# Kernel optimization log

Measured on AMD Instinct MI355X. Metric: run time of the kernel, lower is better.

Reference implementation:

```python
import jax, jax.numpy as jnp
import numpy as np

# Constants from the source's eval path
BBOX_STDS = (0.1, 0.1, 0.2, 0.2)   # cfg.TRAIN.BBOX_NORMALIZE_STDS (MEANS are zeros)
PRE_NMS = 300                       # cfg.TEST.RPN_POST_NMS_TOP_N
POST_K = 100                        # cfg.PERSON_NMS (fixed output size; zero-padded)
NMS_THRESH = 0.3
SCORE_THRESH = 0.05


def setup_inputs() -> dict:
    key = jax.random.key(0)
    k1, k2, k3, k4 = jax.random.split(key, 4)
    B, N = 64, 32768
    H = W = 1024.0
    # plausible RPN proposal boxes inside the image
    xy = jax.random.uniform(k1, (B, N, 2)) * (W - 160.0)
    wh = jax.random.uniform(k2, (B, N, 2)) * 120.0 + 8.0
    boxes = jnp.concatenate([xy, xy + wh], axis=-1)          # [B,N,4] x1y1x2y2
    cls_prob = jax.random.uniform(k3, (B, N, 2))              # softmax probs [bg, person]
    box_deltas = jax.random.normal(k4, (B, N, 4)) * 0.5
    im_info = jnp.tile(jnp.array([H, W, 1.0], jnp.float32), (B, 1))
    return {"cls_prob": cls_prob, "boxes": boxes, "box_deltas": box_deltas, "im_info": im_info}


def _decode_and_clip(boxes, deltas, im_info):
    # bbox_transform_inv with de-normalized deltas, then clip_boxes
    stds = jnp.array(BBOX_STDS, boxes.dtype)
    d = deltas * stds                                         # MEANS are zero
    w = boxes[..., 2] - boxes[..., 0] + 1.0
    h = boxes[..., 3] - boxes[..., 1] + 1.0
    cx = boxes[..., 0] + 0.5 * w
    cy = boxes[..., 1] + 0.5 * h
    pcx = d[..., 0] * w + cx
    pcy = d[..., 1] * h + cy
    pw = jnp.exp(d[..., 2]) * w
    ph = jnp.exp(d[..., 3]) * h
    x1 = pcx - 0.5 * pw
    y1 = pcy - 0.5 * ph
    x2 = pcx + 0.5 * pw
    y2 = pcy + 0.5 * ph
    hmax = im_info[:, 0][:, None] - 1.0   # [B,1]
    wmax = im_info[:, 1][:, None] - 1.0
    x1 = jnp.clip(x1, 0.0, wmax)
    y1 = jnp.clip(y1, 0.0, hmax)
    x2 = jnp.clip(x2, 0.0, wmax)
    y2 = jnp.clip(y2, 0.0, hmax)
    return jnp.stack([x1, y1, x2, y2], axis=-1)               # [B,N,4]


def _nms_single(boxes_i, scores_i):
    # threshold -> sort (top-k) -> greedy NMS -> fixed-size padded output
    valid = scores_i >= SCORE_THRESH
    s = jnp.where(valid, scores_i, -jnp.inf)
    topv, topi = jax.lax.top_k(s, PRE_NMS)                    # descending sort + pre_nms_topN
    b = boxes_i[topi]                                          # [M,4]
    x1, y1, x2, y2 = b[:, 0], b[:, 1], b[:, 2], b[:, 3]
    areas = (x2 - x1 + 1.0) * (y2 - y1 + 1.0)
    xx1 = jnp.maximum(x1[:, None], x1[None, :])
    yy1 = jnp.maximum(y1[:, None], y1[None, :])
    xx2 = jnp.minimum(x2[:, None], x2[None, :])
    yy2 = jnp.minimum(y2[:, None], y2[None, :])
    inter = jnp.maximum(xx2 - xx1 + 1.0, 0.0) * jnp.maximum(yy2 - yy1 + 1.0, 0.0)
    iou = inter / (areas[:, None] + areas[None, :] - inter)    # [M,M]
    iou = jax.lax.stop_gradient(iou)                           # only drives the boolean keep mask
    idx = jnp.arange(PRE_NMS)
    keep0 = jnp.isfinite(topv)                                 # drop below-threshold padding

    def body(i, keep):
        sup = (iou[i] > NMS_THRESH) & (idx > i) & keep[i]
        return keep & ~sup

    keep = jax.lax.fori_loop(0, PRE_NMS, body, keep0)
    # compact kept boxes (in score order) into a fixed [POST_K,4] buffer, zero-padded
    rank = jnp.cumsum(keep) - 1
    dst = jnp.where(keep & (rank < POST_K), rank, POST_K)      # overflow row POST_K is discarded
    out = jnp.zeros((POST_K + 1, 4), b.dtype).at[dst].set(b)
    return out[:POST_K]


def reference(cls_prob, boxes, box_deltas, im_info):
    pred = _decode_and_clip(boxes, box_deltas, im_info)        # [B,N,4]
    scores_person = cls_prob[:, :, 1]                          # person column
    kept = jax.vmap(_nms_single)(pred, scores_person)          # [B,POST_K,4]
    B = pred.shape[0]
    bidx = jnp.broadcast_to(jnp.arange(B, dtype=pred.dtype)[:, None, None], (B, POST_K, 1))
    return jnp.concatenate([bidx, kept], axis=-1)              # [B,POST_K,5] rois
```

## Files before the change

### kernel.cpp

```cpp
#include <hip/hip_runtime.h>
#include <cstdint>
#include <cstddef>

#define PRE_NMS  300
#define POST_K   100
#define NBUCKET  4096
#define CAND_MAX 2048
#define NCHUNK   16
#define SUB      128
#define NWORDS   5
#define KCAP     192
#define KW       3
#define SUP_STRIDE 8
#define NBUK     512
#define MBASE    0xC0800000u
#define NMS_T    0.3f
#define SCORE_T  0.05f
#define FAST_T   0.9875f

typedef unsigned long long u64;

__device__ __forceinline__ float4 decode_box(float4 bo, float4 de,
                                             float wmax, float hmax) {
    float w  = bo.z - bo.x + 1.0f;
    float hh = bo.w - bo.y + 1.0f;
    float cx = bo.x + 0.5f * w;
    float cy = bo.y + 0.5f * hh;
    float pcx = de.x * 0.1f * w + cx;
    float pcy = de.y * 0.1f * hh + cy;
    float pw  = expf(de.z * 0.2f) * w;
    float ph  = expf(de.w * 0.2f) * hh;
    float x1 = fminf(fmaxf(pcx - 0.5f * pw, 0.0f), wmax);
    float y1 = fminf(fmaxf(pcy - 0.5f * ph, 0.0f), hmax);
    float x2 = fminf(fmaxf(pcx + 0.5f * pw, 0.0f), wmax);
    float y2 = fminf(fmaxf(pcy + 0.5f * ph, 0.0f), hmax);
    return make_float4(x1, y1, x2, y2);
}

__global__ __launch_bounds__(256) void scan_kernel(
    const float* __restrict__ cls_prob,
    const float* __restrict__ boxes,
    const float* __restrict__ deltas,
    const float* __restrict__ im_info,
    u64* __restrict__ keyG,
    float4* __restrict__ boxG,
    int* __restrict__ cntG,
    int N)
{
    const int b     = blockIdx.x >> 4;
    const int chunk = blockIdx.x & (NCHUNK - 1);
    const int nq    = N / 2;
    const int per   = (nq + NCHUNK - 1) / NCHUNK;
    const int base  = chunk * per;
    const int end   = min(base + per, nq);

    __shared__ int lcnt;
    __shared__ u64 lk[SUB];
    __shared__ float4 lb[SUB];
    if (threadIdx.x == 0) lcnt = 0;
    __syncthreads();

    const float hmax = im_info[b * 3 + 0] - 1.0f;
    const float wmax = im_info[b * 3 + 1] - 1.0f;
    const float4* cp = (const float4*)(cls_prob + (size_t)b * N * 2);
    for (int q = base + threadIdx.x; q < end; q += 256) {
        float4 v = cp[q];
        #pragma unroll
        for (int h = 0; h < 2; ++h) {
            float s = h ? v.w : v.y;
            if (s >= FAST_T) {
                int pos = atomicAdd(&lcnt, 1);
                if (pos < SUB) {
                    int idx = 2 * q + h;
                    unsigned int m = __float_as_uint(s) ^ 0xFFFFFFFFu;
                    float4 bo = *(const float4*)(boxes  + ((size_t)b * N + idx) * 4);
                    float4 de = *(const float4*)(deltas + ((size_t)b * N + idx) * 4);
                    lk[pos] = ((u64)m << 32) | (unsigned int)idx;
                    lb[pos] = decode_box(bo, de, wmax, hmax);
                }
            }
        }
    }
    __syncthreads();

    const int cnt = lcnt;
    const size_t obase = (size_t)b * NCHUNK + chunk;
    u64* kb = keyG + obase * SUB;
    float4* bbo = boxG + obase * SUB;
    for (int i = threadIdx.x; i < min(cnt, SUB); i += 256) {
        kb[i]  = lk[i];
        bbo[i] = lb[i];
    }
    if (threadIdx.x == 0) cntG[obase] = cnt;
}

__device__ __forceinline__ u64 keep_init_word(int Kv, int w) {
    int rem = Kv - 64 * w;
    if (rem >= 64) return ~0ull;
    if (rem <= 0)  return 0ull;
    return (1ull << rem) - 1ull;
}

__device__ __forceinline__ u64 bits_above(int b) {
    return (b == 63) ? 0ull : (~0ull << (b + 1));
}

__device__ __forceinline__ int key_bucket(u64 key) {
    unsigned int m = (unsigned int)(key >> 32);
    int d = (int)(m - MBASE);
    if (d < 0) return 0;
    int bu = d >> 9;
    return (bu > NBUK - 1) ? (NBUK - 1) : bu;
}

__device__ __forceinline__ float box_area(float4 v) {
    return (v.z - v.x + 1.0f) * (v.w - v.y + 1.0f);
}

__global__ __launch_bounds__(512) void proposal_kernel(
    const float* __restrict__ cls_prob,
    const float* __restrict__ boxes,
    const float* __restrict__ deltas,
    const float* __restrict__ im_info,
    float* __restrict__ out,
    const u64* __restrict__ keyG,
    const float4* __restrict__ boxG,
    const int* __restrict__ cntG,
    int useWS, int N)
{
    const int b   = blockIdx.x;
    const int tid = threadIdx.x;
    const int NT  = 512;

    __shared__ u64 cand[CAND_MAX];
    int* hist4k = (int*)cand;
    int* buk_off = (int*)cand;
    int* buk_cnt = buk_off + NBUK;
    __shared__ float4 bb[PRE_NMS];
    __shared__ u64 supRow[PRE_NMS * SUP_STRIDE];
    u64* skey2 = supRow;
    __shared__ u64 keepw[NWORDS];
    __shared__ int sel[POST_K];
    __shared__ int ws8[8];
    __shared__ int n_out;
    __shared__ int need_full;
    __shared__ int sh_cc;
    __shared__ int sh_ok;
    __shared__ int cand_count;
    __shared__ int cutoff;
    __shared__ int ccnt[NCHUNK], coff[NCHUNK + 1];

    if (tid == 0) { cand_count = 0; need_full = 0; }
    __syncthreads();

    const float4* cp = (const float4*)(cls_prob + (size_t)b * N * 2);
    const int nq = N / 2;
    const float hmax = im_info[b * 3 + 0] - 1.0f;
    const float wmax = im_info[b * 3 + 1] - 1.0f;

    if (useWS && tid < NCHUNK) ccnt[tid] = cntG[b * NCHUNK + tid];
    __syncthreads();
    if (tid == 0) {
        int ok = useWS;
        int tot = 0;
        if (useWS) {
            for (int c = 0; c < NCHUNK; ++c) {
                if (ccnt[c] > SUB) ok = 0;
                coff[c] = tot;
                tot += ccnt[c];
            }
            coff[NCHUNK] = tot;
            if (tot < PRE_NMS || tot > NT) ok = 0;
        }
        sh_ok = ok;
        sh_cc = tot;
    }
    __syncthreads();
    const bool fast = (sh_ok != 0);
    int cc;

    if (fast) {
        cc = sh_cc;
        buk_off[tid] = 0;
        buk_cnt[tid] = 0;
        if (tid < PRE_NMS) bb[tid] = make_float4(0.f, 0.f, 0.f, 0.f);
        __syncthreads();

        const bool have = (tid < cc);
        u64 my = 0; float4 mybox = make_float4(0.f, 0.f, 0.f, 0.f);
        int bu = 0;
        if (have) {
            int ch = 0;
            while (ch < NCHUNK - 1 && coff[ch + 1] <= tid) ++ch;
            size_t p = ((size_t)b * NCHUNK + ch) * SUB + (tid - coff[ch]);
            my = keyG[p];
            mybox = boxG[p];
            bu = key_bucket(my);
            atomicAdd(&buk_off[bu], 1);
        }
        __syncthreads();
        {
            int v = buk_off[tid];
            int lane = tid & 63;
            int incl = v;
            #pragma unroll
            for (int d = 1; d < 64; d <<= 1) {
                int nv = __shfl_up(incl, d, 64);
                if (lane >= d) incl += nv;
            }
            if (lane == 63) ws8[tid >> 6] = incl;
            __syncthreads();
            int woff = 0;
            #pragma unroll
            for (int w = 0; w < 8; ++w)
                if (w < (tid >> 6)) woff += ws8[w];
            __syncthreads();
            buk_off[tid] = woff + incl - v;
        }
        __syncthreads();
        if (have) skey2[buk_off[bu] + atomicAdd(&buk_cnt[bu], 1)] = my;
        __syncthreads();
        if (have) {
            int o = buk_off[bu], n = buk_cnt[bu];
            int r = o;
            for (int t = o; t < o + n; ++t) r += (skey2[t] < my) ? 1 : 0;
            if (r < PRE_NMS) bb[r] = mybox;
        }
        __syncthreads();
    } else {
        for (int q = tid; q < nq; q += NT) {
            float4 v = cp[q];
            #pragma unroll
            for (int h = 0; h < 2; ++h) {
                float s = h ? v.w : v.y;
                if (s >= FAST_T) {
                    int pos = atomicAdd(&cand_count, 1);
                    if (pos < CAND_MAX) {
                        unsigned int m = __float_as_uint(s) ^ 0xFFFFFFFFu;
                        cand[pos] = ((u64)m << 32) | (unsigned int)(2 * q + h);
                    }
                }
            }
        }
        __syncthreads();
        if (cand_count < PRE_NMS) {
            for (int i = tid; i < NBUCKET; i += NT) hist4k[i] = 0;
            __syncthreads();
            for (int q = tid; q < nq; q += NT) {
                float4 v = cp[q];
                if (v.y >= SCORE_T) atomicAdd(&hist4k[min((int)(v.y * (float)NBUCKET), NBUCKET - 1)], 1);
                if (v.w >= SCORE_T) atomicAdd(&hist4k[min((int)(v.w * (float)NBUCKET), NBUCKET - 1)], 1);
            }
            __syncthreads();
            if (tid == 0) {
                int acc = 0, c = 0;
                for (int i = NBUCKET - 1; i >= 0; --i) {
                    acc += hist4k[i];
                    if (acc >= PRE_NMS) { c = i; break; }
                }
                cutoff = c;
                cand_count = 0;
            }
            __syncthreads();
            const int c = cutoff;
            for (int q = tid; q < nq; q += NT) {
                float4 v = cp[q];
                #pragma unroll
                for (int h = 0; h < 2; ++h) {
                    float s = h ? v.w : v.y;
                    if (s >= SCORE_T) {
                        int bu = min((int)(s * (float)NBUCKET), NBUCKET - 1);
                        if (bu >= c) {
                            int pos = atomicAdd(&cand_count, 1);
                            if (pos < CAND_MAX) {
                                unsigned int m = __float_as_uint(s) ^ 0xFFFFFFFFu;
                                cand[pos] = ((u64)m << 32) | (unsigned int)(2 * q + h);
                            }
                        }
                    }
                }
            }
            __syncthreads();
        }
        cc = min(cand_count, CAND_MAX);
        if (tid == 0) sh_cc = cc;
        __syncthreads();
        cc = sh_cc;
        if (tid < PRE_NMS) bb[tid] = make_float4(0.f, 0.f, 0.f, 0.f);
        __syncthreads();
        for (int c2 = tid; c2 < cc; c2 += NT) {
            u64 my = cand[c2];
            int r = 0;
            for (int k = 0; k < cc; ++k) r += (cand[k] < my) ? 1 : 0;
            if (r < PRE_NMS) {
                int idx = (int)(my & 0xFFFFFFFFull);
                float4 bo = *(const float4*)(boxes  + ((size_t)b * N + idx) * 4);
                float4 de = *(const float4*)(deltas + ((size_t)b * N + idx) * 4);
                bb[r] = decode_box(bo, de, wmax, hmax);
            }
        }
        __syncthreads();
    }

    const int Kv = min(cc, PRE_NMS);

    {
        const int lane = tid & 63;
        const int wv   = tid >> 6;
        float4 cb[KW]; float ca[KW];
        #pragma unroll
        for (int g = 0; g < KW; ++g) {
            float4 v = bb[g * 64 + lane];
            cb[g] = v;
            ca[g] = box_area(v);
        }
        for (int i = wv; i < KCAP; i += 8) {
            float4 bi = bb[i];
            float ai = box_area(bi);
            const int wi = i >> 6, bbit = i & 63;
            u64* rp = supRow + (size_t)i * SUP_STRIDE;
            #pragma unroll
            for (int g = 0; g < KW; ++g) {
                u64 word = 0;
                if (g >= wi) {
                    float xx1 = fmaxf(bi.x, cb[g].x);
                    float yy1 = fmaxf(bi.y, cb[g].y);
                    float xx2 = fminf(bi.z, cb[g].z);
                    float yy2 = fminf(bi.w, cb[g].w);
                    float iw = fmaxf(xx2 - xx1 + 1.0f, 0.0f);
                    float ih = fmaxf(yy2 - yy1 + 1.0f, 0.0f);
                    float inter = iw * ih;
                    bool ov = (inter > NMS_T * (ai + ca[g] - inter));
                    u64 bal = __ballot(ov);
                    word = (g == wi) ? (bal & bits_above(bbit)) : bal;
                }
                if (lane == 0) rp[g] = word;
            }
        }
    }
    __syncthreads();

    if (tid < 64) {
        u64 kw0 = keep_init_word(Kv, 0);
        u64 kw1 = keep_init_word(Kv, 1);
        u64 kw2 = keep_init_word(Kv, 2);

        int nk = 0;
        #pragma unroll
        for (int wi = 0; wi < KW; ++wi) {
            if (nk >= POST_K) break;
            u64 w = (wi == 0) ? kw0 : (wi == 1) ? kw1 : kw2;
            while (w != 0ull && nk < POST_K) {
                int b1 = __ffsll(w) - 1;
                u64 w1 = w & bits_above(b1);
                int b2 = (w1 != 0ull) ? (__ffsll(w1) - 1) : -1;
                u64 w2 = (b2 >= 0) ? (w1 & bits_above(b2)) : 0ull;
                int b3 = (w2 != 0ull) ? (__ffsll(w2) - 1) : -1;
                u64 w3 = (b3 >= 0) ? (w2 & bits_above(b3)) : 0ull;
                int b4 = (w3 != 0ull) ? (__ffsll(w3) - 1) : -1;

                const int base = wi * 64;
                const u64* p1 = supRow + (size_t)(base + b1) * SUP_STRIDE;
                const u64* p2 = supRow + (size_t)(base + ((b2 >= 0) ? b2 : b1)) * SUP_STRIDE;
                const u64* p3 = supRow + (size_t)(base + ((b3 >= 0) ? b3 : b1)) * SUP_STRIDE;
                const u64* p4 = supRow + (size_t)(base + ((b4 >= 0) ? b4 : b1)) * SUP_STRIDE;
                u64 a0 = p1[0], a1 = p1[1], a2 = p1[2];
                u64 c0 = p2[0], c1 = p2[1], c2 = p2[2];
                u64 d0 = p3[0], d1 = p3[1], d2 = p3[2];
                u64 e0 = p4[0], e1 = p4[1], e2 = p4[2];

                u64 aw = (wi == 0) ? a0 : (wi == 1) ? a1 : a2;
                u64 cw = (wi == 0) ? c0 : (wi == 1) ? c1 : c2;
                u64 dw = (wi == 0) ? d0 : (wi == 1) ? d1 : d2;

                kw0 &= ~a0; kw1 &= ~a1; kw2 &= ~a2;
                ++nk;
                bool k2 = false, k3 = false;
                if (b2 >= 0 && nk < POST_K && !((aw >> b2) & 1ull)) {
                    kw0 &= ~c0; kw1 &= ~c1; kw2 &= ~c2;
                    ++nk; k2 = true;
                }
                if (b3 >= 0 && nk < POST_K && !((aw >> b3) & 1ull)
                    && !(k2 && ((cw >> b3) & 1ull))) {
                    kw0 &= ~d0; kw1 &= ~d1; kw2 &= ~d2;
                    ++nk; k3 = true;
                }
                if (b4 >= 0 && nk < POST_K && !((aw >> b4) & 1ull)
                    && !(k2 && ((cw >> b4) & 1ull))
                    && !(k3 && ((dw >> b4) & 1ull))) {
                    kw0 &= ~e0; kw1 &= ~e1; kw2 &= ~e2;
                    ++nk;
                }
                int blast = (b4 >= 0) ? b4 : ((b3 >= 0) ? b3 : ((b2 >= 0) ? b2 : b1));
                u64 self = (wi == 0) ? kw0 : (wi == 1) ? kw1 : kw2;
                w = self & bits_above(blast);
            }
        }
        if (tid == 0) {
            keepw[0] = kw0; keepw[1] = kw1; keepw[2] = kw2;
            keepw[3] = 0ull; keepw[4] = 0ull;
            n_out = nk;
            need_full = (nk < POST_K && Kv > KCAP) ? 1 : 0;
        }
    }
    __syncthreads();

    if (need_full) {
        for (int t = tid; t < PRE_NMS * NWORDS; t += NT) {
            int w = t / PRE_NMS;
            int i = t - w * PRE_NMS;
            int jbase = w * 64;
            int jend  = min(jbase + 64, PRE_NMS);
            u64 bits = 0;
            int jstart = max(jbase, i + 1);
            if (jstart < jend) {
                float4 bi = bb[i];
                float ai = box_area(bi);
                for (int j = jstart; j < jend; ++j) {
                    float4 bj = bb[j];
                    float aj = box_area(bj);
                    float xx1 = fmaxf(bi.x, bj.x);
                    float yy1 = fmaxf(bi.y, bj.y);
                    float xx2 = fminf(bi.z, bj.z);
                    float yy2 = fminf(bi.w, bj.w);
                    float iw = fmaxf(xx2 - xx1 + 1.0f, 0.0f);
                    float ih = fmaxf(yy2 - yy1 + 1.0f, 0.0f);
                    float inter = iw * ih;
                    if (inter > NMS_T * (ai + aj - inter)) bits |= (1ull << (j - jbase));
                }
            }
            supRow[i * SUP_STRIDE + w] = bits;
        }
        __syncthreads();
        if (tid == 0) {
            u64 kk[NWORDS];
            #pragma unroll
            for (int w = 0; w < NWORDS; ++w) kk[w] = keep_init_word(Kv, w);
            int nk = 0;
            for (int i = 0; i < PRE_NMS && nk < POST_K; ++i) {
                if ((kk[i >> 6] >> (i & 63)) & 1ull) {
                    const u64* r = supRow + (size_t)i * SUP_STRIDE;
                    #pragma unroll
                    for (int w = 0; w < NWORDS; ++w) kk[w] &= ~r[w];
                    ++nk;
                }
            }
            #pragma unroll
            for (int w = 0; w < NWORDS; ++w) keepw[w] = kk[w];
            n_out = nk;
        }
        __syncthreads();
    }

    if (tid < PRE_NMS) {
        int wi = tid >> 6, bi = tid & 63;
        u64 w = keepw[wi];
        int prefix = 0;
        #pragma unroll
        for (int ww = 0; ww < NWORDS; ++ww)
            if (ww < wi) prefix += __popcll(keepw[ww]);
        prefix += __popcll(w & ((1ull << bi) - 1ull));
        if (((w >> bi) & 1ull) && prefix < POST_K) sel[prefix] = tid;
    }
    __syncthreads();

    if (tid < POST_K) {
        float* op = out + ((size_t)b * POST_K + tid) * 5;
        op[0] = (float)b;
        if (tid < n_out) {
            float4 v = bb[sel[tid]];
            op[1] = v.x; op[2] = v.y; op[3] = v.z; op[4] = v.w;
        } else {
            op[1] = 0.0f; op[2] = 0.0f; op[3] = 0.0f; op[4] = 0.0f;
        }
    }
}

extern "C" void kernel_launch(void* const* d_in, const int* in_sizes, int n_in,
                              void* d_out, int out_size, void* d_ws, size_t ws_size,
                              hipStream_t stream) {
    const float* cls_prob = (const float*)d_in[0];
    const float* boxes    = (const float*)d_in[1];
    const float* deltas   = (const float*)d_in[2];
    const float* im_info  = (const float*)d_in[3];
    float* out = (float*)d_out;

    const int B = in_sizes[3] / 3;
    const int N = in_sizes[0] / (B * 2);

    const size_t nSlots = (size_t)B * NCHUNK * SUB;
    int*    cntG = (int*)d_ws;
    u64*    keyG = (u64*)((char*)d_ws + 16384);
    float4* boxG = (float4*)((char*)d_ws + 16384 + nSlots * sizeof(u64));
    size_t need = 16384 + nSlots * (sizeof(u64) + sizeof(float4));
    int useWS   = (ws_size >= need && B * NCHUNK * (int)sizeof(int) <= 16384) ? 1 : 0;

    if (useWS) {
        scan_kernel<<<B * NCHUNK, 256, 0, stream>>>(cls_prob, boxes, deltas, im_info,
                                                    keyG, boxG, cntG, N);
    }
    proposal_kernel<<<B, 512, 0, stream>>>(cls_prob, boxes, deltas, im_info, out,
                                           keyG, boxG, cntG, useWS, N);
}
```

Baseline: 127.5 us.

## Replace serial greedy NMS scan with parallel fixed-point column iteration

Result: faster. 117.9 us (-7.5%).

```diff
diff --git a/kernel.cpp b/kernel.cpp
--- a/kernel.cpp
+++ b/kernel.cpp
@@ -101,10 +101,6 @@
     return (1ull << rem) - 1ull;
 }
 
-__device__ __forceinline__ u64 bits_above(int b) {
-    return (b == 63) ? 0ull : (~0ull << (b + 1));
-}
-
 __device__ __forceinline__ int key_bucket(u64 key) {
     unsigned int m = (unsigned int)(key >> 32);
     int d = (int)(m - MBASE);
@@ -139,6 +135,7 @@
     __shared__ float4 bb[PRE_NMS];
     __shared__ u64 supRow[PRE_NMS * SUP_STRIDE];
     u64* skey2 = supRow;
+    u64* colW  = supRow;
     __shared__ u64 keepw[NWORDS];
     __shared__ int sel[POST_K];
     __shared__ int ws8[8];
@@ -314,92 +311,68 @@
             cb[g] = v;
             ca[g] = box_area(v);
         }
-        for (int i = wv; i < KCAP; i += 8) {
-            float4 bi = bb[i];
-            float ai = box_area(bi);
-            const int wi = i >> 6, bbit = i & 63;
-            u64* rp = supRow + (size_t)i * SUP_STRIDE;
+        for (int j = wv; j < KCAP; j += 8) {
+            float4 bj = bb[j];
+            float aj = box_area(bj);
+            const int jw = j >> 6, jb = j & 63;
+            u64* cpw = colW + (size_t)j * 4;
             #pragma unroll
             for (int g = 0; g < KW; ++g) {
                 u64 word = 0;
-                if (g >= wi) {
-                    float xx1 = fmaxf(bi.x, cb[g].x);
-                    float yy1 = fmaxf(bi.y, cb[g].y);
-                    float xx2 = fminf(bi.z, cb[g].z);
-                    float yy2 = fminf(bi.w, cb[g].w);
+                if (g <= jw) {
+                    float xx1 = fmaxf(bj.x, cb[g].x);
+                    float yy1 = fmaxf(bj.y, cb[g].y);
+                    float xx2 = fminf(bj.z, cb[g].z);
+                    float yy2 = fminf(bj.w, cb[g].w);
                     float iw = fmaxf(xx2 - xx1 + 1.0f, 0.0f);
                     float ih = fmaxf(yy2 - yy1 + 1.0f, 0.0f);
                     float inter = iw * ih;
-                    bool ov = (inter > NMS_T * (ai + ca[g] - inter));
+                    bool ov = (inter > NMS_T * (aj + ca[g] - inter));
                     u64 bal = __ballot(ov);
-                    word = (g == wi) ? (bal & bits_above(bbit)) : bal;
-                }
-                if (lane == 0) rp[g] = word;
+                    word = (g == jw) ? (bal & ((1ull << jb) - 1ull)) : bal;
+                }
+                if (lane == 0) cpw[g] = word;
             }
         }
     }
     __syncthreads();
 
     if (tid < 64) {
-        u64 kw0 = keep_init_word(Kv, 0);
-        u64 kw1 = keep_init_word(Kv, 1);
-        u64 kw2 = keep_init_word(Kv, 2);
-
-        int nk = 0;
-        #pragma unroll
-        for (int wi = 0; wi < KW; ++wi) {
-            if (nk >= POST_K) break;
-            u64 w = (wi == 0) ? kw0 : (wi == 1) ? kw1 : kw2;
-            while (w != 0ull && nk < POST_K) {
-                int b1 = __ffsll(w) - 1;
-                u64 w1 = w & bits_above(b1);
-                int b2 = (w1 != 0ull) ? (__ffsll(w1) - 1) : -1;
-                u64 w2 = (b2 >= 0) ? (w1 & bits_above(b2)) : 0ull;
-                int b3 = (w2 != 0ull) ? (__ffsll(w2) - 1) : -1;
-                u64 w3 = (b3 >= 0) ? (w2 & bits_above(b3)) : 0ull;
-                int b4 = (w3 != 0ull) ? (__ffsll(w3) - 1) : -1;
-
-                const int base = wi * 64;
-                const u64* p1 = supRow + (size_t)(base + b1) * SUP_STRIDE;
-                const u64* p2 = supRow + (size_t)(base + ((b2 >= 0) ? b2 : b1)) * SUP_STRIDE;
-                const u64* p3 = supRow + (size_t)(base + ((b3 >= 0) ? b3 : b1)) * SUP_STRIDE;
-                const u64* p4 = supRow + (size_t)(base + ((b4 >= 0) ? b4 : b1)) * SUP_STRIDE;
-                u64 a0 = p1[0], a1 = p1[1], a2 = p1[2];
-                u64 c0 = p2[0], c1 = p2[1], c2 = p2[2];
-                u64 d0 = p3[0], d1 = p3[1], d2 = p3[2];
-                u64 e0 = p4[0], e1 = p4[1], e2 = p4[2];
-
-                u64 aw = (wi == 0) ? a0 : (wi == 1) ? a1 : a2;
-                u64 cw = (wi == 0) ? c0 : (wi == 1) ? c1 : c2;
-                u64 dw = (wi == 0) ? d0 : (wi == 1) ? d1 : d2;
-
-                kw0 &= ~a0; kw1 &= ~a1; kw2 &= ~a2;
-                ++nk;
-                bool k2 = false, k3 = false;
-                if (b2 >= 0 && nk < POST_K && !((aw >> b2) & 1ull)) {
-                    kw0 &= ~c0; kw1 &= ~c1; kw2 &= ~c2;
-                    ++nk; k2 = true;
-                }
-                if (b3 >= 0 && nk < POST_K && !((aw >> b3) & 1ull)
-                    && !(k2 && ((cw >> b3) & 1ull))) {
-                    kw0 &= ~d0; kw1 &= ~d1; kw2 &= ~d2;
-                    ++nk; k3 = true;
-                }
-                if (b4 >= 0 && nk < POST_K && !((aw >> b4) & 1ull)
-                    && !(k2 && ((cw >> b4) & 1ull))
-                    && !(k3 && ((dw >> b4) & 1ull))) {
-                    kw0 &= ~e0; kw1 &= ~e1; kw2 &= ~e2;
-                    ++nk;
-                }
-                int blast = (b4 >= 0) ? b4 : ((b3 >= 0) ? b3 : ((b2 >= 0) ? b2 : b1));
-                u64 self = (wi == 0) ? kw0 : (wi == 1) ? kw1 : kw2;
-                w = self & bits_above(blast);
-            }
-        }
-        if (tid == 0) {
-            keepw[0] = kw0; keepw[1] = kw1; keepw[2] = kw2;
+        const int lane = tid;
+        u64 c00 = colW[(size_t)lane * 4 + 0];
+        u64 c10 = colW[(size_t)(64 + lane) * 4 + 0];
+        u64 c11 = colW[(size_t)(64 + lane) * 4 + 1];
+        u64 c20 = colW[(size_t)(128 + lane) * 4 + 0];
+        u64 c21 = colW[(size_t)(128 + lane) * 4 + 1];
+        u64 c22 = colW[(size_t)(128 + lane) * 4 + 2];
+
+        u64 kv0 = keep_init_word(Kv, 0);
+        u64 kv1 = keep_init_word(Kv, 1);
+        u64 kv2 = keep_init_word(Kv, 2);
+        bool v0 = (kv0 >> lane) & 1ull;
+        bool v1 = (kv1 >> lane) & 1ull;
+        bool v2 = (kv2 >> lane) & 1ull;
+        bool b0 = v0, b1 = v1, b2 = v2;
+
+        for (int it = 0; it < KCAP + 8; ++it) {
+            u64 w0 = __ballot(b0);
+            u64 w1 = __ballot(b1);
+            u64 w2 = __ballot(b2);
+            bool n0 = v0 && (((w0 & c00)) == 0ull);
+            bool n1 = v1 && (((w0 & c10) | (w1 & c11)) == 0ull);
+            bool n2 = v2 && (((w0 & c20) | (w1 & c21) | (w2 & c22)) == 0ull);
+            u64 ch = __ballot(n0 != b0 || n1 != b1 || n2 != b2);
+            b0 = n0; b1 = n1; b2 = n2;
+            if (ch == 0ull) break;
+        }
+        u64 f0 = __ballot(b0);
+        u64 f1 = __ballot(b1);
+        u64 f2 = __ballot(b2);
+        if (lane == 0) {
+            keepw[0] = f0; keepw[1] = f1; keepw[2] = f2;
             keepw[3] = 0ull; keepw[4] = 0ull;
-            n_out = nk;
+            int nk = __popcll(f0) + __popcll(f1) + __popcll(f2);
+            n_out = (nk < POST_K) ? nk : POST_K;
             need_full = (nk < POST_K && Kv > KCAP) ? 1 : 0;
         }
     }
```
